# Optimization experiments

Measured on AMD Instinct MI355X. Metric: run time of the kernel, lower is better.

## Reference

```python
import jax, jax.numpy as jnp
import numpy as np

LOG_HALF = float(np.log(0.5))  # log_g(0) = log(relu(0)+0.5) = log(0.5)

def log_g(x):
    # log of g(x) = where(x>=0, x+0.5, sigmoid(x))
    return jnp.where(x >= 0.0, jnp.log(jnp.maximum(x, 0.0) + 0.5), -jax.nn.softplus(-x))

def setup_inputs() -> dict:
    key = jax.random.key(0)
    k1, k2, k3, k4 = jax.random.split(key, 4)
    B, T, D, E = 4, 4096, 1024, 1536
    x = jax.random.normal(k1, (B, T, D), dtype=jnp.float32)
    W_f = jax.random.normal(k2, (2 * E, D), dtype=jnp.float32) * 0.02
    b_f = jax.random.normal(k3, (2 * E,), dtype=jnp.float32) * 0.02
    W_down = jax.random.normal(k4, (D, E), dtype=jnp.float32) * 0.02
    return {"x": x, "W_f": W_f, "b_f": b_f, "W_down": W_down}

def reference(x, W_f, b_f, W_down):
    B, T, D = x.shape
    E = W_down.shape[1]
    # fused input projection, split into gate pre-act k and candidate pre-act h_x
    kz, h_x = jnp.split(jnp.einsum('btd,ed->bte', x, W_f) + b_f, 2, axis=-1)
    log_z = -jax.nn.softplus(-kz)          # log sigmoid(k)
    log_coeffs = -jax.nn.softplus(kz)      # log (1 - sigmoid(k))
    log_tilde_h = log_g(h_x)
    # prepend initial log hidden state log_g(0) = log 0.5
    log_h0 = jnp.full((B, 1, E), LOG_HALF, dtype=x.dtype)
    log_values = jnp.concatenate([log_h0, log_tilde_h + log_z], axis=1)  # (B, T+1, E)
    # a_star = pad(cumsum(log_coeffs), one zero row at front along time)
    a_star = jnp.concatenate(
        [jnp.zeros((B, 1, E), dtype=x.dtype), jnp.cumsum(log_coeffs, axis=1)], axis=1)
    log_h = a_star + jax.lax.cumlogsumexp(log_values - a_star, axis=1)
    h = jnp.exp(log_h)[:, 1:]              # (B, T, E)
    return jnp.einsum('bte,de->btd', h, W_down)
```

## Files before the change

### kernel.cpp

```cpp
#include <hip/hip_runtime.h>
#include <hip/hip_bf16.h>
#include <stdint.h>


typedef __bf16 bf16x8 __attribute__((ext_vector_type(8)));
typedef float  f32x4  __attribute__((ext_vector_type(4)));

__device__ __forceinline__ uint16_t f32_to_bf16(float f) {
  union { float f; uint32_t u; } v; v.f = f;
  uint32_t r = (v.u + 0x7FFFu + ((v.u >> 16) & 1u)) >> 16;
  return (uint16_t)r;
}
__device__ __forceinline__ float bf16_to_f32(uint16_t u) {
  union { uint32_t u; float f; } v; v.u = ((uint32_t)u) << 16;
  return v.f;
}

__device__ __forceinline__ void gload_lds16(const uint16_t* g, uint16_t* l) {
  __builtin_amdgcn_global_load_lds(
      (__attribute__((address_space(1))) void*)(g),
      (__attribute__((address_space(3))) void*)(l), 16, 0, 0);
}

__global__ __launch_bounds__(256) void cast_f32_bf16(
    const float* __restrict__ in, uint16_t* __restrict__ out, int n4) {
  int i = blockIdx.x * blockDim.x + threadIdx.x;
  if (i >= n4) return;
  float4 v = reinterpret_cast<const float4*>(in)[i];
  ushort4 o;
  o.x = f32_to_bf16(v.x); o.y = f32_to_bf16(v.y);
  o.z = f32_to_bf16(v.z); o.w = f32_to_bf16(v.w);
  reinterpret_cast<ushort4*>(out)[i] = o;
}

template <int OUT_BF16_BIAS>
__global__ __launch_bounds__(512, 2) void gemm256(
    const uint16_t* __restrict__ A, const uint16_t* __restrict__ Bt,
    const float* __restrict__ bias, void* __restrict__ Cout,
    int M, int N, int K) {
  __shared__ alignas(16) uint16_t lds[4 * 16384];

  const int tid  = threadIdx.x;
  const int wave = tid >> 6;
  const int lane = tid & 63;
  const int wr = wave >> 2;
  const int wc = wave & 3;

  const int bid = (int)blockIdx.x;
  const int xq  = bid & 7;
  const int j   = bid >> 3;
  const int pi  = xq + ((j >> 3) << 3);
  const int q   = j & 7;
  const int mt  = ((pi & 31) << 1) + (q >> 2);
  const int nt  = ((pi >> 5) << 2) + (q & 3);
  const int m0  = mt << 8;
  const int n0  = nt << 8;

  const int NT = K >> 5;

  const int srow = wave * 16 + (lane >> 2);
  const int skg  = (lane & 3) ^ ((lane >> 3) & 3);
  const uint16_t* Ag0 = A  + (size_t)(m0 + srow) * K + skg * 8;
  const uint16_t* Ag1 = A  + (size_t)(m0 + 128 + srow) * K + skg * 8;
  const uint16_t* Bg0 = Bt + (size_t)(n0 + srow) * K + skg * 8;
  const uint16_t* Bg1 = Bt + (size_t)(n0 + 128 + srow) * K + skg * 8;
  const int sdw = wave * 512;

  const int kgq = (lane >> 4) ^ ((lane >> 1) & 3);
  const int rA = (wr * 128 + (lane & 15)) * 32 + kgq * 8;
  const int rB = (wc * 64  + (lane & 15)) * 32 + kgq * 8;

  f32x4 acc[8][4] = {};

#pragma unroll
  for (int tt = 0; tt < 3; ++tt) {
    uint16_t* sb = &lds[tt * 16384];
    gload_lds16(Ag0 + tt * 32, sb + sdw);
    gload_lds16(Ag1 + tt * 32, sb + 4096 + sdw);
    gload_lds16(Bg0 + tt * 32, sb + 8192 + sdw);
    gload_lds16(Bg1 + tt * 32, sb + 12288 + sdw);
  }

  for (int u = 0; u < NT; ++u) {
    const uint16_t* Ab = &lds[(u & 3) * 16384 + rA];
    const uint16_t* Bb = &lds[(u & 3) * 16384 + 8192 + rB];
    const int us = (u + 3 < NT) ? (u + 3) : (NT - 1);
    uint16_t* sb = &lds[((u + 3) & 3) * 16384];
    const size_t kofs = (size_t)us * 32;

    asm volatile("s_waitcnt vmcnt(8)" ::: "memory");
    __builtin_amdgcn_s_barrier();

    bf16x8 af0[4], af1[4], bfr[4];
#pragma unroll
    for (int m = 0; m < 4; ++m) af0[m] = *reinterpret_cast<const bf16x8*>(Ab + m * 512);
#pragma unroll
    for (int n = 0; n < 4; ++n) bfr[n] = *reinterpret_cast<const bf16x8*>(Bb + n * 512);
    gload_lds16(Ag0 + kofs, sb + sdw);
    gload_lds16(Ag1 + kofs, sb + 4096 + sdw);
    __builtin_amdgcn_sched_barrier(0);
    __builtin_amdgcn_s_barrier();
    asm volatile("s_waitcnt lgkmcnt(0)" ::: "memory");
    __builtin_amdgcn_sched_barrier(0);
    __builtin_amdgcn_s_setprio(1);
#pragma unroll
    for (int m = 0; m < 4; ++m)
#pragma unroll
      for (int n = 0; n < 4; ++n)
        acc[m][n] = __builtin_amdgcn_mfma_f32_16x16x32_bf16(bfr[n], af0[m], acc[m][n], 0, 0, 0);
    __builtin_amdgcn_s_setprio(0);
    __builtin_amdgcn_sched_barrier(0);

#pragma unroll
    for (int m = 0; m < 4; ++m) af1[m] = *reinterpret_cast<const bf16x8*>(Ab + (m + 4) * 512);
    gload_lds16(Bg0 + kofs, sb + 8192 + sdw);
    gload_lds16(Bg1 + kofs, sb + 12288 + sdw);
    __builtin_amdgcn_sched_barrier(0);
    __builtin_amdgcn_s_barrier();
    asm volatile("s_waitcnt lgkmcnt(0)" ::: "memory");
    __builtin_amdgcn_sched_barrier(0);
    __builtin_amdgcn_s_setprio(1);
#pragma unroll
    for (int m = 0; m < 4; ++m)
#pragma unroll
      for (int n = 0; n < 4; ++n)
        acc[m + 4][n] = __builtin_amdgcn_mfma_f32_16x16x32_bf16(bfr[n], af1[m], acc[m + 4][n], 0, 0, 0);
    __builtin_amdgcn_s_setprio(0);
    __builtin_amdgcn_sched_barrier(0);
  }
  asm volatile("s_waitcnt vmcnt(0)" ::: "memory");

  const int r0 = m0 + wr * 128 + (lane & 15);
  const int cb = n0 + wc * 64 + (lane >> 4) * 4;
  if constexpr (OUT_BF16_BIAS) {
    uint16_t* C = (uint16_t*)Cout;
#pragma unroll
    for (int m = 0; m < 8; ++m) {
      const int row = r0 + m * 16;
#pragma unroll
      for (int n = 0; n < 4; ++n) {
        const int col = cb + n * 16;
        ushort4 o;
        o.x = f32_to_bf16(acc[m][n][0] + bias[col + 0]);
        o.y = f32_to_bf16(acc[m][n][1] + bias[col + 1]);
        o.z = f32_to_bf16(acc[m][n][2] + bias[col + 2]);
        o.w = f32_to_bf16(acc[m][n][3] + bias[col + 3]);
        *reinterpret_cast<ushort4*>(&C[(size_t)row * N + col]) = o;
      }
    }
  } else {
    float* C = (float*)Cout;
#pragma unroll
    for (int m = 0; m < 8; ++m) {
      const int row = r0 + m * 16;
#pragma unroll
      for (int n = 0; n < 4; ++n) {
        const int col = cb + n * 16;
        float4 o;
        o.x = acc[m][n][0]; o.y = acc[m][n][1];
        o.z = acc[m][n][2]; o.w = acc[m][n][3];
        *reinterpret_cast<float4*>(&C[(size_t)row * N + col]) = o;
      }
    }
  }
}

__device__ __forceinline__ void gate_val(float kz, float hx, float& a, float& v) {
  float ek = __expf(-fabsf(kz));
  float r  = 1.0f / (1.0f + ek);
  float z  = (kz >= 0.0f) ? r : ek * r;
  a        = (kz >= 0.0f) ? ek * r : r;
  float g;
  if (hx >= 0.0f) {
    g = hx + 0.5f;
  } else {
    float eh = __expf(hx);
    g = eh / (1.0f + eh);
  }
  v = z * g;
}

__global__ __launch_bounds__(256) void scan_pass1(
    const uint16_t* __restrict__ proj, float* __restrict__ Ac,
    float* __restrict__ Vc, int T, int E, int CH, int L) {
  const int e = blockIdx.x * 256 + threadIdx.x;
  const int c = blockIdx.y;
  const int b = blockIdx.z;
  const int N1 = 2 * E;
  const uint16_t* p = proj + (size_t)(b * T + c * L) * N1 + e;
  float A = 1.0f, V = 0.0f;
  for (int t = 0; t < L; ++t) {
    float kz = bf16_to_f32(p[0]);
    float hx = bf16_to_f32(p[E]);
    float a, v; gate_val(kz, hx, a, v);
    A *= a;
    V = a * V + v;
    p += N1;
  }
  const size_t idx = ((size_t)(b * CH + c)) * E + e;
  Ac[idx] = A; Vc[idx] = V;
}

__global__ __launch_bounds__(256) void scan_pass2(
    const float* __restrict__ Ac, const float* __restrict__ Vc,
    float* __restrict__ hstart, int E, int CH) {
  const int e = blockIdx.x * 256 + threadIdx.x;
  const int b = blockIdx.y;
  float h = 0.5f;
  for (int c = 0; c < CH; ++c) {
    const size_t idx = ((size_t)(b * CH + c)) * E + e;
    hstart[idx] = h;
    h = Ac[idx] * h + Vc[idx];
  }
}

__global__ __launch_bounds__(256) void scan_pass3(
    const uint16_t* __restrict__ proj, const float* __restrict__ hstart,
    uint16_t* __restrict__ hout, int T, int E, int CH, int L) {
  const int e = blockIdx.x * 256 + threadIdx.x;
  const int c = blockIdx.y;
  const int b = blockIdx.z;
  const int N1 = 2 * E;
  const uint16_t* p = proj + (size_t)(b * T + c * L) * N1 + e;
  uint16_t* o = hout + (size_t)(b * T + c * L) * E + e;
  float h = hstart[((size_t)(b * CH + c)) * E + e];
  for (int t = 0; t < L; ++t) {
    float kz = bf16_to_f32(p[0]);
    float hx = bf16_to_f32(p[E]);
    float a, v; gate_val(kz, hx, a, v);
    h = a * h + v;
    *o = f32_to_bf16(h);
    p += N1; o += E;
  }
}

extern "C" void kernel_launch(void* const* d_in, const int* in_sizes, int n_in,
                              void* d_out, int out_size, void* d_ws, size_t ws_size,
                              hipStream_t stream) {
  const float* x   = (const float*)d_in[0];
  const float* W_f = (const float*)d_in[1];
  const float* b_f = (const float*)d_in[2];
  const float* W_d = (const float*)d_in[3];
  const int Bb = 4, T = 4096, D = 1024, E = 1536;
  const int M = Bb * T;
  const int N1 = 2 * E;
  const int CH = 64, L = T / CH;

  char* w = (char*)d_ws;
  uint16_t* x_bf  = (uint16_t*)w; w += (size_t)M * D * 2;
  uint16_t* Wf_bf = (uint16_t*)w; w += (size_t)N1 * D * 2;
  uint16_t* Wd_bf = (uint16_t*)w; w += (size_t)D * E * 2;
  uint16_t* proj  = (uint16_t*)w; w += (size_t)M * N1 * 2;
  uint16_t* h_bf  = (uint16_t*)w; w += (size_t)M * E * 2;
  float* Ac     = (float*)w; w += (size_t)Bb * CH * E * 4;
  float* Vc     = (float*)w; w += (size_t)Bb * CH * E * 4;
  float* hstart = (float*)w; w += (size_t)Bb * CH * E * 4;

  cast_f32_bf16<<<M * D / 4 / 256, 256, 0, stream>>>(x, x_bf, M * D / 4);
  cast_f32_bf16<<<N1 * D / 4 / 256, 256, 0, stream>>>(W_f, Wf_bf, N1 * D / 4);
  cast_f32_bf16<<<D * E / 4 / 256, 256, 0, stream>>>(W_d, Wd_bf, D * E / 4);

  gemm256<1><<<(M / 256) * (N1 / 256), 512, 0, stream>>>(
      x_bf, Wf_bf, b_f, proj, M, N1, D);

  scan_pass1<<<dim3(E / 256, CH, Bb), 256, 0, stream>>>(proj, Ac, Vc, T, E, CH, L);
  scan_pass2<<<dim3(E / 256, Bb), 256, 0, stream>>>(Ac, Vc, hstart, E, CH);
  scan_pass3<<<dim3(E / 256, CH, Bb), 256, 0, stream>>>(proj, hstart, h_bf, T, E, CH, L);

  gemm256<0><<<(M / 256) * (D / 256), 512, 0, stream>>>(
      h_bf, Wd_bf, nullptr, d_out, M, D, E);
}
```

Baseline: 283.0 us.

## Interleave gate/candidate columns, fuse casts, and fold chunk-prefix scan into pass3

W_f rows and bias are permuted during casting so the projection output interleaves kz and hx per feature, letting the scan kernels read both with one 32-bit load instead of two strided 16-bit loads. The three cast kernels are merged into one grid-stride launch. The separate chunk-carry kernel is removed, and each pass3 block recomputes its starting state serially from the chunk summaries. Inner scan loops are unrolled by 4. This trades redundant per-block prefix work (up to 63 steps) for one fewer launch and better coalescing of the scan reads.

```diff
diff --git a/kernel.cpp b/kernel.cpp
--- a/kernel.cpp
+++ b/kernel.cpp
@@ -22,15 +22,34 @@
       (__attribute__((address_space(3))) void*)(l), 16, 0, 0);
 }
 
-__global__ __launch_bounds__(256) void cast_f32_bf16(
-    const float* __restrict__ in, uint16_t* __restrict__ out, int n4) {
-  int i = blockIdx.x * blockDim.x + threadIdx.x;
-  if (i >= n4) return;
-  float4 v = reinterpret_cast<const float4*>(in)[i];
+__device__ __forceinline__ void cast4(const float* s, uint16_t* d, int j) {
+  float4 v = reinterpret_cast<const float4*>(s)[j];
   ushort4 o;
   o.x = f32_to_bf16(v.x); o.y = f32_to_bf16(v.y);
   o.z = f32_to_bf16(v.z); o.w = f32_to_bf16(v.w);
-  reinterpret_cast<ushort4*>(out)[i] = o;
+  reinterpret_cast<ushort4*>(d)[j] = o;
+}
+
+__global__ __launch_bounds__(256) void cast_all(
+    const float* __restrict__ x,   uint16_t* __restrict__ x_bf,
+    const float* __restrict__ W_f, uint16_t* __restrict__ Wf_bf,
+    const float* __restrict__ b_f, float* __restrict__ bias_p,
+    const float* __restrict__ W_d, uint16_t* __restrict__ Wd_bf) {
+  const int stride = gridDim.x * blockDim.x;
+  const int gid = blockIdx.x * blockDim.x + threadIdx.x;
+  if (gid < 3072)
+    bias_p[gid] = b_f[(gid & 1) ? 1536 + (gid >> 1) : (gid >> 1)];
+  for (int i = gid; i < 4194304; i += stride) cast4(x, x_bf, i);
+  for (int i = gid; i < 786432; i += stride) {
+    const int r = i >> 8, cg = i & 255;
+    const int rp = (r < 1536) ? (r << 1) : (((r - 1536) << 1) | 1);
+    float4 v = reinterpret_cast<const float4*>(W_f)[i];
+    ushort4 o;
+    o.x = f32_to_bf16(v.x); o.y = f32_to_bf16(v.y);
+    o.z = f32_to_bf16(v.z); o.w = f32_to_bf16(v.w);
+    reinterpret_cast<ushort4*>(Wf_bf)[rp * 256 + cg] = o;
+  }
+  for (int i = gid; i < 393216; i += stride) cast4(W_d, Wd_bf, i);
 }
 
 template <int OUT_BF16_BIAS>
@@ -180,6 +199,12 @@
   v = z * g;
 }
 
+__device__ __forceinline__ void gate_from_u32(uint32_t u, float& a, float& v) {
+  float kz = bf16_to_f32((uint16_t)(u & 0xFFFFu));
+  float hx = bf16_to_f32((uint16_t)(u >> 16));
+  gate_val(kz, hx, a, v);
+}
+
 __global__ __launch_bounds__(256) void scan_pass1(
     const uint16_t* __restrict__ proj, float* __restrict__ Ac,
     float* __restrict__ Vc, int T, int E, int CH, int L) {
@@ -187,12 +212,11 @@
   const int c = blockIdx.y;
   const int b = blockIdx.z;
   const int N1 = 2 * E;
-  const uint16_t* p = proj + (size_t)(b * T + c * L) * N1 + e;
+  const uint16_t* p = proj + (size_t)(b * T + c * L) * N1 + 2 * e;
   float A = 1.0f, V = 0.0f;
+#pragma unroll 4
   for (int t = 0; t < L; ++t) {
-    float kz = bf16_to_f32(p[0]);
-    float hx = bf16_to_f32(p[E]);
-    float a, v; gate_val(kz, hx, a, v);
+    float a, v; gate_from_u32(*reinterpret_cast<const uint32_t*>(p), a, v);
     A *= a;
     V = a * V + v;
     p += N1;
@@ -201,33 +225,24 @@
   Ac[idx] = A; Vc[idx] = V;
 }
 
-__global__ __launch_bounds__(256) void scan_pass2(
-    const float* __restrict__ Ac, const float* __restrict__ Vc,
-    float* __restrict__ hstart, int E, int CH) {
-  const int e = blockIdx.x * 256 + threadIdx.x;
-  const int b = blockIdx.y;
-  float h = 0.5f;
-  for (int c = 0; c < CH; ++c) {
-    const size_t idx = ((size_t)(b * CH + c)) * E + e;
-    hstart[idx] = h;
-    h = Ac[idx] * h + Vc[idx];
-  }
-}
-
 __global__ __launch_bounds__(256) void scan_pass3(
-    const uint16_t* __restrict__ proj, const float* __restrict__ hstart,
-    uint16_t* __restrict__ hout, int T, int E, int CH, int L) {
+    const uint16_t* __restrict__ proj, const float* __restrict__ Ac,
+    const float* __restrict__ Vc, uint16_t* __restrict__ hout,
+    int T, int E, int CH, int L) {
   const int e = blockIdx.x * 256 + threadIdx.x;
   const int c = blockIdx.y;
   const int b = blockIdx.z;
   const int N1 = 2 * E;
-  const uint16_t* p = proj + (size_t)(b * T + c * L) * N1 + e;
+  float h = 0.5f;
+  for (int cc = 0; cc < c; ++cc) {
+    const size_t idx = ((size_t)(b * CH + cc)) * E + e;
+    h = Ac[idx] * h + Vc[idx];
+  }
+  const uint16_t* p = proj + (size_t)(b * T + c * L) * N1 + 2 * e;
   uint16_t* o = hout + (size_t)(b * T + c * L) * E + e;
-  float h = hstart[((size_t)(b * CH + c)) * E + e];
+#pragma unroll 4
   for (int t = 0; t < L; ++t) {
-    float kz = bf16_to_f32(p[0]);
-    float hx = bf16_to_f32(p[E]);
-    float a, v; gate_val(kz, hx, a, v);
+    float a, v; gate_from_u32(*reinterpret_cast<const uint32_t*>(p), a, v);
     h = a * h + v;
     *o = f32_to_bf16(h);
     p += N1; o += E;
@@ -254,18 +269,15 @@
   uint16_t* h_bf  = (uint16_t*)w; w += (size_t)M * E * 2;
   float* Ac     = (float*)w; w += (size_t)Bb * CH * E * 4;
   float* Vc     = (float*)w; w += (size_t)Bb * CH * E * 4;
-  float* hstart = (float*)w; w += (size_t)Bb * CH * E * 4;
-
-  cast_f32_bf16<<<M * D / 4 / 256, 256, 0, stream>>>(x, x_bf, M * D / 4);
-  cast_f32_bf16<<<N1 * D / 4 / 256, 256, 0, stream>>>(W_f, Wf_bf, N1 * D / 4);
-  cast_f32_bf16<<<D * E / 4 / 256, 256, 0, stream>>>(W_d, Wd_bf, D * E / 4);
+  float* bias_p = (float*)w; w += (size_t)N1 * 4;
+
+  cast_all<<<2048, 256, 0, stream>>>(x, x_bf, W_f, Wf_bf, b_f, bias_p, W_d, Wd_bf);
 
   gemm256<1><<<(M / 256) * (N1 / 256), 512, 0, stream>>>(
-      x_bf, Wf_bf, b_f, proj, M, N1, D);
+      x_bf, Wf_bf, bias_p, proj, M, N1, D);
 
   scan_pass1<<<dim3(E / 256, CH, Bb), 256, 0, stream>>>(proj, Ac, Vc, T, E, CH, L);
-  scan_pass2<<<dim3(E / 256, Bb), 256, 0, stream>>>(Ac, Vc, hstart, E, CH);
-  scan_pass3<<<dim3(E / 256, CH, Bb), 256, 0, stream>>>(proj, hstart, h_bf, T, E, CH, L);
+  scan_pass3<<<dim3(E / 256, CH, Bb), 256, 0, stream>>>(proj, Ac, Vc, h_bf, T, E, CH, L);
 
   gemm256<0><<<(M / 256) * (D / 256), 512, 0, stream>>>(
       h_bf, Wd_bf, nullptr, d_out, M, D, E);
```

Result: no change. 283.7 us (+0.3%).
